# Performance work log

Measured on AMD Instinct MI355X. Metric: run time of the kernel, lower is better.

The kernel has to match this reference:

```python
import jax, jax.numpy as jnp
import numpy as np

N, E, IN_DIM, HID = 50000, 800000, 128, 64
NEG_SLOPE = 0.01  # torch F.leaky_relu default


def setup_inputs() -> dict:
    key = jax.random.key(0)
    ks = jax.random.split(key, 8)
    x = jax.random.normal(ks[0], (N, IN_DIM), jnp.float32)
    edge_index = jax.random.randint(ks[1], (2, E), 0, N, dtype=jnp.int32)
    edge_weight = jax.random.uniform(ks[2], (E,), jnp.float32)
    h = jnp.zeros((N, HID), jnp.float32)
    c = jnp.zeros((N, HID), jnp.float32)
    sx = 1.0 / np.sqrt(IN_DIM)
    sh = 1.0 / np.sqrt(HID)
    # gate order along leading axis: [i, f, c(tilde), o]; K=2 Chebyshev weights
    Wx = (jax.random.normal(ks[3], (4, 2, IN_DIM, HID), jnp.float32) * sx)
    bx = jnp.zeros((4, HID), jnp.float32)
    Wh = (jax.random.normal(ks[4], (4, 2, HID, HID), jnp.float32) * sh)
    bh = jnp.zeros((4, HID), jnp.float32)
    wc = jax.random.normal(ks[5], (3, HID), jnp.float32) * 0.1  # peepholes for i, f, o
    bg = jnp.zeros((4, HID), jnp.float32)
    W_head = jax.random.normal(ks[6], (HID, 1), jnp.float32) * sh
    b_head = jnp.zeros((1,), jnp.float32)
    return dict(x=x, edge_index=edge_index, edge_weight=edge_weight, h=h, c=c,
                Wx=Wx, bx=bx, Wh=Wh, bh=bh, wc=wc, bg=bg, W_head=W_head, b_head=b_head)


def _cheb_norm(src, dst, ew, n):
    # ChebConv 'sym' normalization with lambda_max=2: L_hat = -D^{-1/2} A D^{-1/2}
    # (the +1 self-loop from the Laplacian cancels against fill_value=-1)
    deg = jnp.zeros((n,), ew.dtype).at[src].add(ew)
    dinv = jnp.where(deg > 0, 1.0 / jnp.sqrt(jnp.where(deg > 0, deg, 1.0)), 0.0)
    return -dinv[src] * ew * dinv[dst]


def _prop(feat, src, dst, norm, n):
    # T1 = L_hat @ feat via edge gather + segment-sum
    return jax.ops.segment_sum(norm[:, None] * feat[src], dst, num_segments=n)


def reference(x, edge_index, edge_weight, h, c, Wx, bx, Wh, bh, wc, bg, W_head, b_head):
    n = x.shape[0]
    src, dst = edge_index[0], edge_index[1]
    norm = _cheb_norm(src, dst, edge_weight, n)
    Tx = _prop(x, src, dst, norm, n)
    Th = _prop(h, src, dst, norm, n)  # shared across all 4 h-side ChebConvs
    # z[g] = X W[g,0] + (L_hat X) W[g,1] + b  for all gates at once
    z = (jnp.einsum('nd,gdh->gnh', x, Wx[:, 0]) + jnp.einsum('nd,gdh->gnh', Tx, Wx[:, 1]) + bx[:, None, :]
         + jnp.einsum('nd,gdh->gnh', h, Wh[:, 0]) + jnp.einsum('nd,gdh->gnh', Th, Wh[:, 1]) + bh[:, None, :])
    i = jax.nn.sigmoid(z[0] + wc[0] * c + bg[0])
    f = jax.nn.sigmoid(z[1] + wc[1] * c + bg[1])
    g = jnp.tanh(z[2] + bg[2])
    c_new = f * c + i * g
    o = jax.nn.sigmoid(z[3] + wc[2] * c_new + bg[3])
    h_new = o * jnp.tanh(c_new)
    out = jax.nn.leaky_relu(h_new, NEG_SLOPE) @ W_head + b_head
    return out, h_new, c_new
```

## Files before the change

kernel.cpp:

```cpp
#include <hip/hip_runtime.h>
#include <hip/hip_bf16.h>

#define IN_DIM 128
#define HID 64
#define NEG_SLOPE 0.01f
#define CAP 5120

typedef __attribute__((ext_vector_type(8))) short short8;
typedef __attribute__((ext_vector_type(4))) short short4v;
typedef __attribute__((ext_vector_type(4))) float f32x4;
typedef unsigned short ushort_t;
typedef unsigned int uint_t;

__device__ __forceinline__ float fsig(float x) { return 1.f / (1.f + __expf(-x)); }
__device__ __forceinline__ float ftanh(float x) { return 1.f - 2.f / (__expf(2.f * x) + 1.f); }

__device__ __forceinline__ ushort_t f2bf(float f) {
    uint_t u = __float_as_uint(f);
    uint_t r = u + 0x7fffu + ((u >> 16) & 1u);
    return (ushort_t)(r >> 16);
}
__device__ __forceinline__ float bf2f(ushort_t s) { return __uint_as_float(((uint_t)s) << 16); }
__device__ __forceinline__ float bf2f_s(short s) { return bf2f((ushort_t)s); }

__global__ __launch_bounds__(256) void cvt_kernel(
    const float* __restrict__ x, const float* __restrict__ h,
    const float* __restrict__ Wx, const float* __restrict__ Wh,
    uint_t* __restrict__ xb_u, uint_t* __restrict__ hb_u, ushort_t* __restrict__ Wp,
    int N) {
    int tid = blockIdx.x * 256 + threadIdx.x;
    int T = gridDim.x * 256;

    int ncvt = N * 96;
    int nx = N * 64;
    for (int i = tid; i < ncvt; i += T) {
        if (i < nx) {
            float2 v = ((const float2*)x)[i];
            xb_u[i] = (uint_t)f2bf(v.x) | ((uint_t)f2bf(v.y) << 16);
        } else {
            int j = i - nx;
            float2 v = ((const float2*)h)[j];
            hb_u[j] = (uint_t)f2bf(v.x) | ((uint_t)f2bf(v.y) << 16);
        }
    }

    for (int idx = tid; idx < 384 * 256; idx += T) {
        int j = idx & 7;
        int tmp = idx >> 3;
        int lane = tmp & 63;
        int t2 = tmp >> 6;
        int ct = t2 & 15;
        int ks = t2 >> 4;
        int k = ks * 32 + (lane >> 4) * 8 + j;
        int colg = ct * 16 + (lane & 15);
        int g = colg >> 6, hd = colg & 63;
        float v;
        if (k < 128)      v = Wx[((g * 2 + 0) * 128 + k) * 64 + hd];
        else if (k < 192) v = Wh[((g * 2 + 0) * 64 + (k - 128)) * 64 + hd];
        else if (k < 320) v = Wx[((g * 2 + 1) * 128 + (k - 192)) * 64 + hd];
        else              v = Wh[((g * 2 + 1) * 64 + (k - 320)) * 64 + hd];
        Wp[idx] = f2bf(v);
    }
}

__global__ __launch_bounds__(256) void part_kernel(
    const int* __restrict__ src, const int* __restrict__ dst, const float* __restrict__ ew,
    int* __restrict__ cur_d, int* __restrict__ cur_s,
    int2* __restrict__ dpart, int2* __restrict__ spart, int E) {
    __shared__ int hd[256], hs[256];
    int t = threadIdx.x;
    hd[t] = 0; hs[t] = 0;
    __syncthreads();
    int base = blockIdx.x * 2048;
    int sv[8], dv[8]; float wv[8];
#pragma unroll
    for (int it = 0; it < 8; ++it) {
        int e = base + it * 256 + t;
        bool ok = e < E;
        sv[it] = ok ? src[e] : 0;
        dv[it] = ok ? dst[e] : 0;
        wv[it] = ok ? ew[e] : 0.f;
        if (ok) {
            atomicAdd(&hd[dv[it] >> 8], 1);
            atomicAdd(&hs[sv[it] >> 8], 1);
        }
    }
    __syncthreads();
    int nd = hd[t], ns = hs[t];
    __syncthreads();
    if (nd) hd[t] = atomicAdd(&cur_d[t * 16], nd);
    if (ns) hs[t] = atomicAdd(&cur_s[t * 16], ns);
    __syncthreads();
#pragma unroll
    for (int it = 0; it < 8; ++it) {
        int e = base + it * 256 + t;
        if (e < E) {
            int d = dv[it], s = sv[it];
            int bd = d >> 8, bs = s >> 8;
            int pd = atomicAdd(&hd[bd], 1);
            int ps = atomicAdd(&hs[bs], 1);
            dpart[(size_t)bd * CAP + pd] = make_int2(s | ((d & 255) << 16), __float_as_int(wv[it]));
            spart[(size_t)bs * CAP + ps] = make_int2(s & 255, __float_as_int(wv[it]));
        }
    }
}

__global__ __launch_bounds__(256) void deg_kernel(const int2* __restrict__ spart,
                                                  const int* __restrict__ cur_s,
                                                  float* __restrict__ dinv, int N) {
    __shared__ float df[256];
    int t = threadIdx.x, b = blockIdx.x;
    df[t] = 0.f;
    __syncthreads();
    int cnt = cur_s[b * 16];
    for (int i = t; i < cnt; i += 256) {
        int2 r = spart[(size_t)b * CAP + i];
        atomicAdd(&df[r.x & 255], __int_as_float(r.y));
    }
    __syncthreads();
    int g = b * 256 + t;
    if (g < N) {
        float dd = df[t];
        dinv[g] = dd > 0.f ? rsqrtf(dd) : 0.f;
    }
}

__global__ __launch_bounds__(256) void fillb_kernel(const int2* __restrict__ dpart,
                                                    const int* __restrict__ cur_d,
                                                    const float* __restrict__ dinv,
                                                    int* __restrict__ rowptr, int* __restrict__ rowend,
                                                    int2* __restrict__ eprm, int N) {
    __shared__ int c[256], sdata[256], pcur[256];
    __shared__ float dl[256];
    int t = threadIdx.x, b = blockIdx.x;
    c[t] = 0;
    int g = b * 256 + t;
    dl[t] = (g < N) ? dinv[g] : 0.f;
    __syncthreads();
    int cnt = cur_d[b * 16];
    for (int i = t; i < cnt; i += 256) {
        int m = dpart[(size_t)b * CAP + i].x;
        atomicAdd(&c[(m >> 16) & 255], 1);
    }
    __syncthreads();
    sdata[t] = c[t];
    __syncthreads();
    for (int off = 1; off < 256; off <<= 1) {
        int tmp = (t >= off) ? sdata[t - off] : 0;
        __syncthreads();
        sdata[t] += tmp;
        __syncthreads();
    }
    int excl = sdata[t] - c[t];
    pcur[t] = excl;
    if (g < N) {
        rowptr[g] = b * CAP + excl;
        rowend[g] = b * CAP + sdata[t];
    }
    __syncthreads();
    for (int i = t; i < cnt; i += 256) {
        int2 r = dpart[(size_t)b * CAP + i];
        int m = r.x;
        int dlo = (m >> 16) & 255;
        int s = m & 0xffff;
        float w = __int_as_float(r.y);
        int pos = atomicAdd(&pcur[dlo], 1);
        float nrm = -dinv[s] * w * dl[dlo];
        eprm[(size_t)b * CAP + pos] = make_int2(s, __float_as_int(nrm));
    }
}

__global__ __launch_bounds__(256) void gather_kernel(const int* __restrict__ rowptr,
                                                     const int* __restrict__ rowend,
                                                     const int2* __restrict__ eprm,
                                                     const ushort_t* __restrict__ xb,
                                                     const ushort_t* __restrict__ hb,
                                                     ushort_t* __restrict__ Txb,
                                                     ushort_t* __restrict__ Thb, int N) {
    int lane = threadIdx.x & 63;
    int wave = threadIdx.x >> 6;
    int grp = lane >> 4, l16 = lane & 15;
    int node = blockIdx.x * 16 + wave * 4 + grp;
    bool valid = node < N;
    int p = 0, end = 0;
    if (valid) { p = rowptr[node]; end = rowend[node]; }

    float ax[8] = {0.f, 0.f, 0.f, 0.f, 0.f, 0.f, 0.f, 0.f};
    float ah[4] = {0.f, 0.f, 0.f, 0.f};

    int idx0 = p + l16;
    int2 pr = (idx0 < end) ? eprm[idx0] : make_int2(0, 0);

    for (int base = p; base < end; base += 16) {
        int2 cur = pr;
        int nidx = base + 16 + l16;
        if (base + 16 < end) pr = (nidx < end) ? eprm[nidx] : make_int2(0, 0);
        int sv = cur.x;
        float wv = __int_as_float(cur.y);
        int mcount = end - base; if (mcount > 16) mcount = 16;
        int sl0 = grp * 16;
        int j = 0;
        for (; j + 4 <= mcount; j += 4) {
            int s0 = __shfl(sv, sl0 + j + 0), s1 = __shfl(sv, sl0 + j + 1);
            int s2 = __shfl(sv, sl0 + j + 2), s3 = __shfl(sv, sl0 + j + 3);
            float w0 = __shfl(wv, sl0 + j + 0), w1 = __shfl(wv, sl0 + j + 1);
            float w2 = __shfl(wv, sl0 + j + 2), w3 = __shfl(wv, sl0 + j + 3);
            short8 xv0 = *(const short8*)(xb + (size_t)s0 * 128 + l16 * 8);
            short8 xv1 = *(const short8*)(xb + (size_t)s1 * 128 + l16 * 8);
            short8 xv2 = *(const short8*)(xb + (size_t)s2 * 128 + l16 * 8);
            short8 xv3 = *(const short8*)(xb + (size_t)s3 * 128 + l16 * 8);
            short4v hv0 = *(const short4v*)(hb + (size_t)s0 * 64 + l16 * 4);
            short4v hv1 = *(const short4v*)(hb + (size_t)s1 * 64 + l16 * 4);
            short4v hv2 = *(const short4v*)(hb + (size_t)s2 * 64 + l16 * 4);
            short4v hv3 = *(const short4v*)(hb + (size_t)s3 * 64 + l16 * 4);
#pragma unroll
            for (int i = 0; i < 8; ++i)
                ax[i] += w0 * bf2f_s(xv0[i]) + w1 * bf2f_s(xv1[i])
                       + w2 * bf2f_s(xv2[i]) + w3 * bf2f_s(xv3[i]);
#pragma unroll
            for (int i = 0; i < 4; ++i)
                ah[i] += w0 * bf2f_s(hv0[i]) + w1 * bf2f_s(hv1[i])
                       + w2 * bf2f_s(hv2[i]) + w3 * bf2f_s(hv3[i]);
        }
        for (; j < mcount; ++j) {
            int s0 = __shfl(sv, sl0 + j);
            float w0 = __shfl(wv, sl0 + j);
            short8 xv0 = *(const short8*)(xb + (size_t)s0 * 128 + l16 * 8);
            short4v hv0 = *(const short4v*)(hb + (size_t)s0 * 64 + l16 * 4);
#pragma unroll
            for (int i = 0; i < 8; ++i) ax[i] += w0 * bf2f_s(xv0[i]);
#pragma unroll
            for (int i = 0; i < 4; ++i) ah[i] += w0 * bf2f_s(hv0[i]);
        }
    }

    if (valid) {
        short8 tx;
#pragma unroll
        for (int i = 0; i < 8; ++i) tx[i] = (short)f2bf(ax[i]);
        *(short8*)(Txb + (size_t)node * 128 + l16 * 8) = tx;
        short4v th;
#pragma unroll
        for (int i = 0; i < 4; ++i) th[i] = (short)f2bf(ah[i]);
        *(short4v*)(Thb + (size_t)node * 64 + l16 * 4) = th;
    }
}

__global__ __launch_bounds__(256, 4) void fused_mfma(
    const ushort_t* __restrict__ xb, const ushort_t* __restrict__ hb,
    const ushort_t* __restrict__ Txb, const ushort_t* __restrict__ Thb,
    const float* __restrict__ c_in, const ushort_t* __restrict__ Wp,
    const float* __restrict__ bx, const float* __restrict__ bh,
    const float* __restrict__ wc, const float* __restrict__ bg,
    const float* __restrict__ Whead, const float* __restrict__ bhead,
    float* __restrict__ out, int N) {
    __shared__ ushort_t Bs[2][8192];
    int tid = threadIdx.x;
    int lane = tid & 63;
    int wave = tid >> 6;
    int quad = lane >> 4, m = lane & 15;
    int row0 = (blockIdx.x * 4 + wave) * 16;
    int ar = row0 + m; if (ar >= N) ar = N - 1;

    {
        const float4* gsrc = (const float4*)(Wp);
        float4* ldst = (float4*)Bs[0];
#pragma unroll
        for (int i = 0; i < 4; ++i) ldst[tid + 256 * i] = gsrc[tid + 256 * i];
    }

    f32x4 acc[16];
#pragma unroll
    for (int ct = 0; ct < 16; ++ct) {
        int g = ct >> 2, hd = (ct & 3) * 16 + m;
        float b = bx[g * 64 + hd] + bh[g * 64 + hd];
        f32x4 bb = {b, b, b, b};
        acc[ct] = bb;
    }

    int ko = quad * 8;
    __syncthreads();

#pragma unroll
    for (int ks = 0; ks < 12; ++ks) {
        int buf = ks & 1;
        float4 tmp[4];
        if (ks < 11) {
            const float4* gsrc = (const float4*)(Wp + (ks + 1) * 8192);
#pragma unroll
            for (int i = 0; i < 4; ++i) tmp[i] = gsrc[tid + 256 * i];
        }
        const ushort_t* a;
        if (ks < 4)       a = xb  + (size_t)ar * 128 + ks * 32 + ko;
        else if (ks < 6)  a = hb  + (size_t)ar * 64 + (ks - 4) * 32 + ko;
        else if (ks < 10) a = Txb + (size_t)ar * 128 + (ks - 6) * 32 + ko;
        else              a = Thb + (size_t)ar * 64 + (ks - 10) * 32 + ko;
        short8 af = *(const short8*)a;
        const short8* bsp = (const short8*)Bs[buf];
#pragma unroll
        for (int ct = 0; ct < 16; ++ct) {
            short8 bf = bsp[ct * 64 + lane];
            acc[ct] = __builtin_amdgcn_mfma_f32_16x16x32_bf16(af, bf, acc[ct], 0, 0, 0);
        }
        if (ks < 11) {
            float4* ldst = (float4*)Bs[buf ^ 1];
#pragma unroll
            for (int i = 0; i < 4; ++i) ldst[tid + 256 * i] = tmp[i];
            __syncthreads();
        }
    }

    float hp[4] = {0.f, 0.f, 0.f, 0.f};
    float bhv = bhead[0];

#pragma unroll
    for (int hs = 0; hs < 4; ++hs) {
        int hd = hs * 16 + m;
        float wc0 = wc[hd], wc1 = wc[64 + hd], wc2 = wc[128 + hd];
        float bg0 = bg[hd], bg1 = bg[64 + hd], bg2 = bg[128 + hd], bg3 = bg[192 + hd];
        float wh = Whead[hd];
#pragma unroll
        for (int reg = 0; reg < 4; ++reg) {
            int n = row0 + quad * 4 + reg;
            if (n < N) {
                float c_old = c_in[(size_t)n * 64 + hd];
                float zi = acc[0 * 4 + hs][reg];
                float zf = acc[1 * 4 + hs][reg];
                float zg = acc[2 * 4 + hs][reg];
                float zo = acc[3 * 4 + hs][reg];
                float ii = fsig(zi + wc0 * c_old + bg0);
                float ff = fsig(zf + wc1 * c_old + bg1);
                float gg = ftanh(zg + bg2);
                float cn = ff * c_old + ii * gg;
                float oo = fsig(zo + wc2 * cn + bg3);
                float hn = oo * ftanh(cn);
                out[N + (size_t)n * 64 + hd] = hn;
                out[N + (size_t)N * 64 + (size_t)n * 64 + hd] = cn;
                float lr = hn > 0.f ? hn : NEG_SLOPE * hn;
                hp[reg] += lr * wh;
            }
        }
    }
#pragma unroll
    for (int reg = 0; reg < 4; ++reg) {
        float v0 = hp[reg];
#pragma unroll
        for (int mask = 1; mask < 16; mask <<= 1) v0 += __shfl_xor(v0, mask);
        if (m == 0) {
            int n0_ = row0 + quad * 4 + reg;
            if (n0_ < N) out[n0_] = v0 + bhv;
        }
    }
}

extern "C" void kernel_launch(void* const* d_in, const int* in_sizes, int n_in,
                              void* d_out, int out_size, void* d_ws, size_t ws_size,
                              hipStream_t stream) {
    const float* x = (const float*)d_in[0];
    const int* ei = (const int*)d_in[1];
    const float* ew = (const float*)d_in[2];
    const float* h = (const float*)d_in[3];
    const float* c = (const float*)d_in[4];
    const float* Wx = (const float*)d_in[5];
    const float* bx = (const float*)d_in[6];
    const float* Wh = (const float*)d_in[7];
    const float* bh = (const float*)d_in[8];
    const float* wc = (const float*)d_in[9];
    const float* bg = (const float*)d_in[10];
    const float* Whead = (const float*)d_in[11];
    const float* bhead = (const float*)d_in[12];

    int N = in_sizes[0] / IN_DIM;
    int E = in_sizes[1] / 2;
    const int* src = ei;
    const int* dst = ei + E;

    int nbuck = (N + 255) >> 8;

    char* wp = (char*)d_ws;
    auto alloc = [&](size_t bytes) {
        char* p = wp;
        wp += (bytes + 255) & ~(size_t)255;
        return p;
    };
    int* cur = (int*)alloc((size_t)2 * nbuck * 16 * 4);
    int* cur_d = cur;
    int* cur_s = cur + (size_t)nbuck * 16;
    float* dinv = (float*)alloc((size_t)N * 4);
    int* rowptr = (int*)alloc((size_t)N * 4);
    int* rowend = (int*)alloc((size_t)N * 4);
    int2* dpart = (int2*)alloc((size_t)nbuck * CAP * 8);
    int2* spart = (int2*)alloc((size_t)nbuck * CAP * 8);
    int2* eprm = spart;
    ushort_t* xb = (ushort_t*)alloc((size_t)N * 128 * 2);
    ushort_t* hb = (ushort_t*)alloc((size_t)N * 64 * 2);
    ushort_t* Txb = (ushort_t*)alloc((size_t)N * 128 * 2);
    ushort_t* Thb = (ushort_t*)alloc((size_t)N * 64 * 2);
    ushort_t* Wp = (ushort_t*)alloc((size_t)384 * 256 * 2);

    hipMemsetAsync(cur, 0, (size_t)2 * nbuck * 16 * 4, stream);

    part_kernel<<<(E + 2047) / 2048, 256, 0, stream>>>(src, dst, ew, cur_d, cur_s,
                                                       dpart, spart, E);
    cvt_kernel<<<2048, 256, 0, stream>>>(x, h, Wx, Wh, (uint_t*)xb, (uint_t*)hb, Wp, N);
    deg_kernel<<<nbuck, 256, 0, stream>>>(spart, cur_s, dinv, N);
    fillb_kernel<<<nbuck, 256, 0, stream>>>(dpart, cur_d, dinv, rowptr, rowend, eprm, N);
    gather_kernel<<<(N + 15) / 16, 256, 0, stream>>>(rowptr, rowend, eprm, xb, hb, Txb, Thb, N);
    fused_mfma<<<(N + 63) / 64, 256, 0, stream>>>(xb, hb, Txb, Thb, c, Wp, bx, bh, wc, bg,
                                                  Whead, bhead, (float*)d_out, N);
}
```

Measured before the change: 239.4 us.

## Fuse neighbor gather into MFMA gate kernel and merge partition with conversion

The edge gather that builds L_hat·x and L_hat·h now runs inside the MFMA gate kernel. Each 512-thread block gathers 32 nodes into LDS and consumes them directly as A operands, so the Txb/Thb global buffers and one launch go away. The partition and bf16 conversion kernels are merged into a single launch whose block index picks the role. The trade-offs: twice as many blocks each restream the full packed weight matrix, LDS use per block is higher, and an extra LDS reduction is needed for the head output.

After: 253.2 us. 5.8% more time.

```diff
diff --git a/kernel.cpp b/kernel.cpp
--- a/kernel.cpp
+++ b/kernel.cpp
@@ -23,14 +23,58 @@
 __device__ __forceinline__ float bf2f(ushort_t s) { return __uint_as_float(((uint_t)s) << 16); }
 __device__ __forceinline__ float bf2f_s(short s) { return bf2f((ushort_t)s); }
 
-__global__ __launch_bounds__(256) void cvt_kernel(
+__global__ __launch_bounds__(256) void part_kernel(
+    const int* __restrict__ src, const int* __restrict__ dst, const float* __restrict__ ew,
     const float* __restrict__ x, const float* __restrict__ h,
     const float* __restrict__ Wx, const float* __restrict__ Wh,
+    int* __restrict__ cur_d, int* __restrict__ cur_s,
+    int2* __restrict__ dpart, int2* __restrict__ spart,
     uint_t* __restrict__ xb_u, uint_t* __restrict__ hb_u, ushort_t* __restrict__ Wp,
-    int N) {
-    int tid = blockIdx.x * 256 + threadIdx.x;
-    int T = gridDim.x * 256;
-
+    int E, int N, int nbPart) {
+    __shared__ int hd[256], hs[256];
+    int t = threadIdx.x;
+
+    if ((int)blockIdx.x < nbPart) {
+        hd[t] = 0; hs[t] = 0;
+        __syncthreads();
+        int base = blockIdx.x * 2048;
+        int sv[8], dv[8]; float wv[8];
+#pragma unroll
+        for (int it = 0; it < 8; ++it) {
+            int e = base + it * 256 + t;
+            bool ok = e < E;
+            sv[it] = ok ? src[e] : 0;
+            dv[it] = ok ? dst[e] : 0;
+            wv[it] = ok ? ew[e] : 0.f;
+            if (ok) {
+                atomicAdd(&hd[dv[it] >> 8], 1);
+                atomicAdd(&hs[sv[it] >> 8], 1);
+            }
+        }
+        __syncthreads();
+        int nd = hd[t], ns = hs[t];
+        __syncthreads();
+        if (nd) hd[t] = atomicAdd(&cur_d[t * 16], nd);
+        if (ns) hs[t] = atomicAdd(&cur_s[t * 16], ns);
+        __syncthreads();
+#pragma unroll
+        for (int it = 0; it < 8; ++it) {
+            int e = base + it * 256 + t;
+            if (e < E) {
+                int d = dv[it], s = sv[it];
+                int bd = d >> 8, bs = s >> 8;
+                int pd = atomicAdd(&hd[bd], 1);
+                int ps = atomicAdd(&hs[bs], 1);
+                dpart[(size_t)bd * CAP + pd] = make_int2(s | ((d & 255) << 16), __float_as_int(wv[it]));
+                spart[(size_t)bs * CAP + ps] = make_int2(s & 255, __float_as_int(wv[it]));
+            }
+        }
+        return;
+    }
+
+    int cb = blockIdx.x - nbPart;
+    int tid = cb * 256 + t;
+    int T = (gridDim.x - nbPart) * 256;
     int ncvt = N * 96;
     int nx = N * 64;
     for (int i = tid; i < ncvt; i += T) {
@@ -53,55 +97,13 @@
         int ks = t2 >> 4;
         int k = ks * 32 + (lane >> 4) * 8 + j;
         int colg = ct * 16 + (lane & 15);
-        int g = colg >> 6, hd = colg & 63;
+        int g = colg >> 6, hdd = colg & 63;
         float v;
-        if (k < 128)      v = Wx[((g * 2 + 0) * 128 + k) * 64 + hd];
-        else if (k < 192) v = Wh[((g * 2 + 0) * 64 + (k - 128)) * 64 + hd];
-        else if (k < 320) v = Wx[((g * 2 + 1) * 128 + (k - 192)) * 64 + hd];
-        else              v = Wh[((g * 2 + 1) * 64 + (k - 320)) * 64 + hd];
+        if (k < 128)      v = Wx[((g * 2 + 0) * 128 + k) * 64 + hdd];
+        else if (k < 192) v = Wh[((g * 2 + 0) * 64 + (k - 128)) * 64 + hdd];
+        else if (k < 320) v = Wx[((g * 2 + 1) * 128 + (k - 192)) * 64 + hdd];
+        else              v = Wh[((g * 2 + 1) * 64 + (k - 320)) * 64 + hdd];
         Wp[idx] = f2bf(v);
-    }
-}
-
-__global__ __launch_bounds__(256) void part_kernel(
-    const int* __restrict__ src, const int* __restrict__ dst, const float* __restrict__ ew,
-    int* __restrict__ cur_d, int* __restrict__ cur_s,
-    int2* __restrict__ dpart, int2* __restrict__ spart, int E) {
-    __shared__ int hd[256], hs[256];
-    int t = threadIdx.x;
-    hd[t] = 0; hs[t] = 0;
-    __syncthreads();
-    int base = blockIdx.x * 2048;
-    int sv[8], dv[8]; float wv[8];
-#pragma unroll
-    for (int it = 0; it < 8; ++it) {
-        int e = base + it * 256 + t;
-        bool ok = e < E;
-        sv[it] = ok ? src[e] : 0;
-        dv[it] = ok ? dst[e] : 0;
-        wv[it] = ok ? ew[e] : 0.f;
-        if (ok) {
-            atomicAdd(&hd[dv[it] >> 8], 1);
-            atomicAdd(&hs[sv[it] >> 8], 1);
-        }
-    }
-    __syncthreads();
-    int nd = hd[t], ns = hs[t];
-    __syncthreads();
-    if (nd) hd[t] = atomicAdd(&cur_d[t * 16], nd);
-    if (ns) hs[t] = atomicAdd(&cur_s[t * 16], ns);
-    __syncthreads();
-#pragma unroll
-    for (int it = 0; it < 8; ++it) {
-        int e = base + it * 256 + t;
-        if (e < E) {
-            int d = dv[it], s = sv[it];
-            int bd = d >> 8, bs = s >> 8;
-            int pd = atomicAdd(&hd[bd], 1);
-            int ps = atomicAdd(&hs[bs], 1);
-            dpart[(size_t)bd * CAP + pd] = make_int2(s | ((d & 255) << 16), __float_as_int(wv[it]));
-            spart[(size_t)bs * CAP + ps] = make_int2(s & 255, __float_as_int(wv[it]));
-        }
     }
 }
 
@@ -170,186 +172,183 @@
     }
 }
 
-__global__ __launch_bounds__(256) void gather_kernel(const int* __restrict__ rowptr,
-                                                     const int* __restrict__ rowend,
-                                                     const int2* __restrict__ eprm,
-                                                     const ushort_t* __restrict__ xb,
-                                                     const ushort_t* __restrict__ hb,
-                                                     ushort_t* __restrict__ Txb,
-                                                     ushort_t* __restrict__ Thb, int N) {
-    int lane = threadIdx.x & 63;
-    int wave = threadIdx.x >> 6;
-    int grp = lane >> 4, l16 = lane & 15;
-    int node = blockIdx.x * 16 + wave * 4 + grp;
-    bool valid = node < N;
-    int p = 0, end = 0;
-    if (valid) { p = rowptr[node]; end = rowend[node]; }
-
-    float ax[8] = {0.f, 0.f, 0.f, 0.f, 0.f, 0.f, 0.f, 0.f};
-    float ah[4] = {0.f, 0.f, 0.f, 0.f};
-
-    int idx0 = p + l16;
-    int2 pr = (idx0 < end) ? eprm[idx0] : make_int2(0, 0);
-
-    for (int base = p; base < end; base += 16) {
-        int2 cur = pr;
-        int nidx = base + 16 + l16;
-        if (base + 16 < end) pr = (nidx < end) ? eprm[nidx] : make_int2(0, 0);
-        int sv = cur.x;
-        float wv = __int_as_float(cur.y);
-        int mcount = end - base; if (mcount > 16) mcount = 16;
-        int sl0 = grp * 16;
-        int j = 0;
-        for (; j + 4 <= mcount; j += 4) {
-            int s0 = __shfl(sv, sl0 + j + 0), s1 = __shfl(sv, sl0 + j + 1);
-            int s2 = __shfl(sv, sl0 + j + 2), s3 = __shfl(sv, sl0 + j + 3);
-            float w0 = __shfl(wv, sl0 + j + 0), w1 = __shfl(wv, sl0 + j + 1);
-            float w2 = __shfl(wv, sl0 + j + 2), w3 = __shfl(wv, sl0 + j + 3);
-            short8 xv0 = *(const short8*)(xb + (size_t)s0 * 128 + l16 * 8);
-            short8 xv1 = *(const short8*)(xb + (size_t)s1 * 128 + l16 * 8);
-            short8 xv2 = *(const short8*)(xb + (size_t)s2 * 128 + l16 * 8);
-            short8 xv3 = *(const short8*)(xb + (size_t)s3 * 128 + l16 * 8);
-            short4v hv0 = *(const short4v*)(hb + (size_t)s0 * 64 + l16 * 4);
-            short4v hv1 = *(const short4v*)(hb + (size_t)s1 * 64 + l16 * 4);
-            short4v hv2 = *(const short4v*)(hb + (size_t)s2 * 64 + l16 * 4);
-            short4v hv3 = *(const short4v*)(hb + (size_t)s3 * 64 + l16 * 4);
-#pragma unroll
-            for (int i = 0; i < 8; ++i)
-                ax[i] += w0 * bf2f_s(xv0[i]) + w1 * bf2f_s(xv1[i])
-                       + w2 * bf2f_s(xv2[i]) + w3 * bf2f_s(xv3[i]);
-#pragma unroll
-            for (int i = 0; i < 4; ++i)
-                ah[i] += w0 * bf2f_s(hv0[i]) + w1 * bf2f_s(hv1[i])
-                       + w2 * bf2f_s(hv2[i]) + w3 * bf2f_s(hv3[i]);
-        }
-        for (; j < mcount; ++j) {
-            int s0 = __shfl(sv, sl0 + j);
-            float w0 = __shfl(wv, sl0 + j);
-            short8 xv0 = *(const short8*)(xb + (size_t)s0 * 128 + l16 * 8);
-            short4v hv0 = *(const short4v*)(hb + (size_t)s0 * 64 + l16 * 4);
-#pragma unroll
-            for (int i = 0; i < 8; ++i) ax[i] += w0 * bf2f_s(xv0[i]);
-#pragma unroll
-            for (int i = 0; i < 4; ++i) ah[i] += w0 * bf2f_s(hv0[i]);
-        }
-    }
-
-    if (valid) {
-        short8 tx;
-#pragma unroll
-        for (int i = 0; i < 8; ++i) tx[i] = (short)f2bf(ax[i]);
-        *(short8*)(Txb + (size_t)node * 128 + l16 * 8) = tx;
-        short4v th;
-#pragma unroll
-        for (int i = 0; i < 4; ++i) th[i] = (short)f2bf(ah[i]);
-        *(short4v*)(Thb + (size_t)node * 64 + l16 * 4) = th;
-    }
-}
-
-__global__ __launch_bounds__(256, 4) void fused_mfma(
+__global__ __launch_bounds__(512, 6) void gather_fused(
+    const int* __restrict__ rowptr, const int* __restrict__ rowend,
+    const int2* __restrict__ eprm,
     const ushort_t* __restrict__ xb, const ushort_t* __restrict__ hb,
-    const ushort_t* __restrict__ Txb, const ushort_t* __restrict__ Thb,
     const float* __restrict__ c_in, const ushort_t* __restrict__ Wp,
     const float* __restrict__ bx, const float* __restrict__ bh,
     const float* __restrict__ wc, const float* __restrict__ bg,
     const float* __restrict__ Whead, const float* __restrict__ bhead,
     float* __restrict__ out, int N) {
     __shared__ ushort_t Bs[2][8192];
+    __shared__ ushort_t Ts[32][200];
+    __shared__ float hsum[32];
+
     int tid = threadIdx.x;
     int lane = tid & 63;
     int wave = tid >> 6;
-    int quad = lane >> 4, m = lane & 15;
-    int row0 = (blockIdx.x * 4 + wave) * 16;
-    int ar = row0 + m; if (ar >= N) ar = N - 1;
+    int grp = lane >> 4, l16 = lane & 15;
+    int nb = blockIdx.x * 32;
 
     {
         const float4* gsrc = (const float4*)(Wp);
         float4* ldst = (float4*)Bs[0];
-#pragma unroll
-        for (int i = 0; i < 4; ++i) ldst[tid + 256 * i] = gsrc[tid + 256 * i];
-    }
-
-    f32x4 acc[16];
-#pragma unroll
-    for (int ct = 0; ct < 16; ++ct) {
-        int g = ct >> 2, hd = (ct & 3) * 16 + m;
-        float b = bx[g * 64 + hd] + bh[g * 64 + hd];
+        ldst[tid] = gsrc[tid];
+        ldst[tid + 512] = gsrc[tid + 512];
+    }
+
+    {
+        int lr = wave * 4 + grp;
+        int node = nb + lr;
+        bool valid = node < N;
+        int p = 0, end = 0;
+        if (valid) { p = rowptr[node]; end = rowend[node]; }
+
+        float ax[8] = {0.f, 0.f, 0.f, 0.f, 0.f, 0.f, 0.f, 0.f};
+        float ah[4] = {0.f, 0.f, 0.f, 0.f};
+
+        int idx0 = p + l16;
+        int2 pr = (idx0 < end) ? eprm[idx0] : make_int2(0, 0);
+        int sl0 = grp * 16;
+
+        for (int base = p; base < end; base += 16) {
+            int2 cur = pr;
+            int nidx = base + 16 + l16;
+            if (base + 16 < end) pr = (nidx < end) ? eprm[nidx] : make_int2(0, 0);
+            int sv = cur.x;
+            float wv = __int_as_float(cur.y);
+            int mcount = end - base; if (mcount > 16) mcount = 16;
+            int j = 0;
+            for (; j + 4 <= mcount; j += 4) {
+                int s0 = __shfl(sv, sl0 + j + 0), s1 = __shfl(sv, sl0 + j + 1);
+                int s2 = __shfl(sv, sl0 + j + 2), s3 = __shfl(sv, sl0 + j + 3);
+                float w0 = __shfl(wv, sl0 + j + 0), w1 = __shfl(wv, sl0 + j + 1);
+                float w2 = __shfl(wv, sl0 + j + 2), w3 = __shfl(wv, sl0 + j + 3);
+                short8 xv0 = *(const short8*)(xb + (size_t)s0 * 128 + l16 * 8);
+                short8 xv1 = *(const short8*)(xb + (size_t)s1 * 128 + l16 * 8);
+                short8 xv2 = *(const short8*)(xb + (size_t)s2 * 128 + l16 * 8);
+                short8 xv3 = *(const short8*)(xb + (size_t)s3 * 128 + l16 * 8);
+                short4v hv0 = *(const short4v*)(hb + (size_t)s0 * 64 + l16 * 4);
+                short4v hv1 = *(const short4v*)(hb + (size_t)s1 * 64 + l16 * 4);
+                short4v hv2 = *(const short4v*)(hb + (size_t)s2 * 64 + l16 * 4);
+                short4v hv3 = *(const short4v*)(hb + (size_t)s3 * 64 + l16 * 4);
+#pragma unroll
+                for (int i = 0; i < 8; ++i)
+                    ax[i] += w0 * bf2f_s(xv0[i]) + w1 * bf2f_s(xv1[i])
+                           + w2 * bf2f_s(xv2[i]) + w3 * bf2f_s(xv3[i]);
+#pragma unroll
+                for (int i = 0; i < 4; ++i)
+                    ah[i] += w0 * bf2f_s(hv0[i]) + w1 * bf2f_s(hv1[i])
+                           + w2 * bf2f_s(hv2[i]) + w3 * bf2f_s(hv3[i]);
+            }
+            for (; j < mcount; ++j) {
+                int s0 = __shfl(sv, sl0 + j);
+                float w0 = __shfl(wv, sl0 + j);
+                short8 xv0 = *(const short8*)(xb + (size_t)s0 * 128 + l16 * 8);
+                short4v hv0 = *(const short4v*)(hb + (size_t)s0 * 64 + l16 * 4);
+#pragma unroll
+                for (int i = 0; i < 8; ++i) ax[i] += w0 * bf2f_s(xv0[i]);
+#pragma unroll
+                for (int i = 0; i < 4; ++i) ah[i] += w0 * bf2f_s(hv0[i]);
+            }
+        }
+
+        short8 tx;
+#pragma unroll
+        for (int i = 0; i < 8; ++i) tx[i] = (short)f2bf(ax[i]);
+        *(short8*)(&Ts[lr][l16 * 8]) = tx;
+        short4v th;
+#pragma unroll
+        for (int i = 0; i < 4; ++i) th[i] = (short)f2bf(ah[i]);
+        *(short4v*)(&Ts[lr][128 + l16 * 4]) = th;
+    }
+
+    int rg = wave >> 2;
+    int hsw = wave & 3;
+    int quad = lane >> 4, m = lane & 15;
+    int ko = quad * 8;
+    int hd = hsw * 16 + m;
+    int ar = nb + rg * 16 + m; if (ar >= N) ar = N - 1;
+
+    f32x4 acc[4];
+#pragma unroll
+    for (int g4 = 0; g4 < 4; ++g4) {
+        float b = bx[g4 * 64 + hd] + bh[g4 * 64 + hd];
         f32x4 bb = {b, b, b, b};
-        acc[ct] = bb;
-    }
-
-    int ko = quad * 8;
+        acc[g4] = bb;
+    }
+
     __syncthreads();
 
 #pragma unroll
     for (int ks = 0; ks < 12; ++ks) {
         int buf = ks & 1;
-        float4 tmp[4];
+        float4 tmp0, tmp1;
         if (ks < 11) {
             const float4* gsrc = (const float4*)(Wp + (ks + 1) * 8192);
-#pragma unroll
-            for (int i = 0; i < 4; ++i) tmp[i] = gsrc[tid + 256 * i];
-        }
-        const ushort_t* a;
-        if (ks < 4)       a = xb  + (size_t)ar * 128 + ks * 32 + ko;
-        else if (ks < 6)  a = hb  + (size_t)ar * 64 + (ks - 4) * 32 + ko;
-        else if (ks < 10) a = Txb + (size_t)ar * 128 + (ks - 6) * 32 + ko;
-        else              a = Thb + (size_t)ar * 64 + (ks - 10) * 32 + ko;
-        short8 af = *(const short8*)a;
+            tmp0 = gsrc[tid];
+            tmp1 = gsrc[tid + 512];
+        }
+        short8 af;
+        if (ks < 4)       af = *(const short8*)(xb + (size_t)ar * 128 + ks * 32 + ko);
+        else if (ks < 6)  af = *(const short8*)(hb + (size_t)ar * 64 + (ks - 4) * 32 + ko);
+        else if (ks < 10) af = *(const short8*)(&Ts[rg * 16 + m][(ks - 6) * 32 + ko]);
+        else              af = *(const short8*)(&Ts[rg * 16 + m][128 + (ks - 10) * 32 + ko]);
         const short8* bsp = (const short8*)Bs[buf];
 #pragma unroll
-        for (int ct = 0; ct < 16; ++ct) {
-            short8 bf = bsp[ct * 64 + lane];
-            acc[ct] = __builtin_amdgcn_mfma_f32_16x16x32_bf16(af, bf, acc[ct], 0, 0, 0);
+        for (int g4 = 0; g4 < 4; ++g4) {
+            short8 bf = bsp[(g4 * 4 + hsw) * 64 + lane];
+            acc[g4] = __builtin_amdgcn_mfma_f32_16x16x32_bf16(af, bf, acc[g4], 0, 0, 0);
         }
         if (ks < 11) {
             float4* ldst = (float4*)Bs[buf ^ 1];
-#pragma unroll
-            for (int i = 0; i < 4; ++i) ldst[tid + 256 * i] = tmp[i];
+            ldst[tid] = tmp0;
+            ldst[tid + 512] = tmp1;
             __syncthreads();
         }
     }
 
+    if (tid < 32) hsum[tid] = 0.f;
+    float bhv = bhead[0];
+    float wc0 = wc[hd], wc1 = wc[64 + hd], wc2 = wc[128 + hd];
+    float bg0 = bg[hd], bg1 = bg[64 + hd], bg2 = bg[128 + hd], bg3 = bg[192 + hd];
+    float wh = Whead[hd];
     float hp[4] = {0.f, 0.f, 0.f, 0.f};
-    float bhv = bhead[0];
-
-#pragma unroll
-    for (int hs = 0; hs < 4; ++hs) {
-        int hd = hs * 16 + m;
-        float wc0 = wc[hd], wc1 = wc[64 + hd], wc2 = wc[128 + hd];
-        float bg0 = bg[hd], bg1 = bg[64 + hd], bg2 = bg[128 + hd], bg3 = bg[192 + hd];
-        float wh = Whead[hd];
-#pragma unroll
-        for (int reg = 0; reg < 4; ++reg) {
-            int n = row0 + quad * 4 + reg;
-            if (n < N) {
-                float c_old = c_in[(size_t)n * 64 + hd];
-                float zi = acc[0 * 4 + hs][reg];
-                float zf = acc[1 * 4 + hs][reg];
-                float zg = acc[2 * 4 + hs][reg];
-                float zo = acc[3 * 4 + hs][reg];
-                float ii = fsig(zi + wc0 * c_old + bg0);
-                float ff = fsig(zf + wc1 * c_old + bg1);
-                float gg = ftanh(zg + bg2);
-                float cn = ff * c_old + ii * gg;
-                float oo = fsig(zo + wc2 * cn + bg3);
-                float hn = oo * ftanh(cn);
-                out[N + (size_t)n * 64 + hd] = hn;
-                out[N + (size_t)N * 64 + (size_t)n * 64 + hd] = cn;
-                float lr = hn > 0.f ? hn : NEG_SLOPE * hn;
-                hp[reg] += lr * wh;
-            }
-        }
-    }
+
+#pragma unroll
+    for (int reg = 0; reg < 4; ++reg) {
+        int n = nb + rg * 16 + quad * 4 + reg;
+        if (n < N) {
+            float c_old = c_in[(size_t)n * 64 + hd];
+            float zi = acc[0][reg];
+            float zf = acc[1][reg];
+            float zg = acc[2][reg];
+            float zo = acc[3][reg];
+            float ii = fsig(zi + wc0 * c_old + bg0);
+            float ff = fsig(zf + wc1 * c_old + bg1);
+            float gg = ftanh(zg + bg2);
+            float cn = ff * c_old + ii * gg;
+            float oo = fsig(zo + wc2 * cn + bg3);
+            float hn = oo * ftanh(cn);
+            out[N + (size_t)n * 64 + hd] = hn;
+            out[N + (size_t)N * 64 + (size_t)n * 64 + hd] = cn;
+            float lrk = hn > 0.f ? hn : NEG_SLOPE * hn;
+            hp[reg] = lrk * wh;
+        }
+    }
+    __syncthreads();
 #pragma unroll
     for (int reg = 0; reg < 4; ++reg) {
         float v0 = hp[reg];
 #pragma unroll
         for (int mask = 1; mask < 16; mask <<= 1) v0 += __shfl_xor(v0, mask);
-        if (m == 0) {
-            int n0_ = row0 + quad * 4 + reg;
-            if (n0_ < N) out[n0_] = v0 + bhv;
-        }
+        if (m == 0) atomicAdd(&hsum[rg * 16 + quad * 4 + reg], v0);
+    }
+    __syncthreads();
+    if (tid < 32) {
+        int n = nb + tid;
+        if (n < N) out[n] = hsum[tid] + bhv;
     }
 }
 
@@ -376,6 +375,7 @@
     const int* dst = ei + E;
 
     int nbuck = (N + 255) >> 8;
+    int nbPart = (E + 2047) / 2048;
 
     char* wp = (char*)d_ws;
     auto alloc = [&](size_t bytes) {
@@ -394,18 +394,16 @@
     int2* eprm = spart;
     ushort_t* xb = (ushort_t*)alloc((size_t)N * 128 * 2);
     ushort_t* hb = (ushort_t*)alloc((size_t)N * 64 * 2);
-    ushort_t* Txb = (ushort_t*)alloc((size_t)N * 128 * 2);
-    ushort_t* Thb = (ushort_t*)alloc((size_t)N * 64 * 2);
     ushort_t* Wp = (ushort_t*)alloc((size_t)384 * 256 * 2);
 
     hipMemsetAsync(cur, 0, (size_t)2 * nbuck * 16 * 4, stream);
 
-    part_kernel<<<(E + 2047) / 2048, 256, 0, stream>>>(src, dst, ew, cur_d, cur_s,
-                                                       dpart, spart, E);
-    cvt_kernel<<<2048, 256, 0, stream>>>(x, h, Wx, Wh, (uint_t*)xb, (uint_t*)hb, Wp, N);
+    part_kernel<<<2048, 256, 0, stream>>>(src, dst, ew, x, h, Wx, Wh,
+                                          cur_d, cur_s, dpart, spart,
+                                          (uint_t*)xb, (uint_t*)hb, Wp, E, N, nbPart);
     deg_kernel<<<nbuck, 256, 0, stream>>>(spart, cur_s, dinv, N);
     fillb_kernel<<<nbuck, 256, 0, stream>>>(dpart, cur_d, dinv, rowptr, rowend, eprm, N);
-    gather_kernel<<<(N + 15) / 16, 256, 0, stream>>>(rowptr, rowend, eprm, xb, hb, Txb, Thb, N);
-    fused_mfma<<<(N + 63) / 64, 256, 0, stream>>>(xb, hb, Txb, Thb, c, Wp, bx, bh, wc, bg,
-                                                  Whead, bhead, (float*)d_out, N);
-}
+    gather_fused<<<(N + 31) / 32, 512, 0, stream>>>(rowptr, rowend, eprm, xb, hb,
+                                                    c, Wp, bx, bh, wc, bg,
+                                                    Whead, bhead, (float*)d_out, N);
+}
```
